# Performance work log

Hardware: AMD Instinct MI355X
Metric: run time of the kernel (lower is better)

The kernel has to match this reference:

```python
import jax, jax.numpy as jnp
import numpy as np

N_TOKENS = 131072
N_E = 1024
E_DIM = 256
BETA = 0.25
GAMMA = 0.99


def setup_inputs() -> dict:
    key = jax.random.key(0)
    k1, k2 = jax.random.split(key)
    z = jax.random.normal(k1, (N_TOKENS, E_DIM), dtype=jnp.float32)
    # nn.Embedding weight init: uniform(-1/n_e, 1/n_e)
    emb_weight = jax.random.uniform(k2, (N_E, E_DIM), dtype=jnp.float32,
                                    minval=-1.0 / N_E, maxval=1.0 / N_E)
    n_mat = jnp.ones((1, N_E), dtype=jnp.float32)
    m_mat = jnp.ones((N_E, E_DIM), dtype=jnp.float32)
    return {"z": z, "emb_weight": emb_weight, "n_mat": n_mat, "m_mat": m_mat,
            "batch_size": 128, "n_train": 100000}


def reference(z, emb_weight, n_mat, m_mat, batch_size, n_train):
    n_e, e_dim = emb_weight.shape
    zf = z.reshape(-1, e_dim)  # (N, e_dim)

    # squared-distance matrix: ||z||^2 + ||e||^2 - 2 z e^T  -> (N, n_e)
    d = (jnp.sum(zf * zf, axis=1, keepdims=True)
         + jnp.sum(emb_weight * emb_weight, axis=1)
         - 2.0 * (zf @ emb_weight.T))
    idx = jnp.argmin(d, axis=1)                       # (N,)
    min_encodings = jax.nn.one_hot(idx, n_e, dtype=z.dtype)  # (N, n_e)

    # z_q = one_hot @ weight == gather
    z_q = emb_weight[idx].reshape(z.shape)

    # EMA codebook update (the Python per-codeword loop == segment reductions)
    counts = jnp.sum(min_encodings, axis=0)           # (n_e,)
    new_n_mat = n_mat * GAMMA + counts[None, :] * (1.0 - GAMMA)
    sums = jax.ops.segment_sum(zf, idx, num_segments=n_e)  # (n_e, e_dim)
    new_m_mat = GAMMA * m_mat + (1.0 - GAMMA) * sums
    new_emb_weight = new_m_mat / new_n_mat[0][:, None]

    commit_loss = BETA * jnp.mean((jax.lax.stop_gradient(z_q) - z) ** 2)
    quant_loss = jnp.mean((z_q - jax.lax.stop_gradient(z)) ** 2)
    z_q_st = z + jax.lax.stop_gradient(z_q - z)       # straight-through

    e_mean = counts / zf.shape[0]
    perplexity = jnp.exp(-jnp.sum(e_mean * jnp.log(e_mean + 1e-10)))

    return (quant_loss, commit_loss, z_q_st, perplexity, min_encodings,
            idx[:, None], new_emb_weight, new_n_mat, new_m_mat)
```

## Files before the change

### kernel.cpp

```cpp
#include <hip/hip_runtime.h>


#define NT 131072
#define NE 1024
#define ED 256

typedef _Float16 f16;
typedef f16  f16x8 __attribute__((ext_vector_type(8)));
typedef float f32x4 __attribute__((ext_vector_type(4)));

static const size_t OFF_QL   = 0;
static const size_t OFF_CL   = 1;
static const size_t OFF_ZQ   = 2;
static const size_t OFF_PPL  = 33554434ULL;
static const size_t OFF_OH   = 33554435ULL;
static const size_t OFF_IDX  = 167772163ULL;
static const size_t OFF_NEMB = 167903235ULL;
static const size_t OFF_NN   = 168165379ULL;
static const size_t OFF_NM   = 168166403ULL;

__device__ __forceinline__ void gload_lds16(const void* g, void* l) {
  __builtin_amdgcn_global_load_lds(
      (const __attribute__((address_space(1))) unsigned int*)g,
      (__attribute__((address_space(3))) unsigned int*)l, 16, 0, 0);
}

__global__ __launch_bounds__(256) void rownorm_k(const float* __restrict__ x,
                                                 float* __restrict__ o, int nrows) {
  int wid  = blockIdx.x * 4 + (threadIdx.x >> 6);
  int lane = threadIdx.x & 63;
  if (wid >= nrows) return;
  float4 v = ((const float4*)(x + (size_t)wid * ED))[lane];
  float s = v.x * v.x + v.y * v.y + v.z * v.z + v.w * v.w;
  #pragma unroll
  for (int off = 32; off; off >>= 1) s += __shfl_down(s, off, 64);
  if (lane == 0) o[wid] = s;
}

__global__ __launch_bounds__(256) void eprep_k(const float* __restrict__ emb,
                                               char* __restrict__ eswz) {
  const int t  = threadIdx.x;
  const int c  = blockIdx.x * 8 + (t >> 5);
  const int kq = t & 31;
  const float* er = emb + (size_t)c * ED + kq * 8;
  float4 v0 = ((const float4*)er)[0];
  float4 v1 = ((const float4*)er)[1];
  float vv[8] = {v0.x, v0.y, v0.z, v0.w, v1.x, v1.y, v1.z, v1.w};
  f16x8 h;
  #pragma unroll
  for (int i = 0; i < 8; ++i) h[i] = (f16)(vv[i] * 1024.0f);
  const int tile = c >> 5, cl = c & 31;
  const int g = (cl << 5) | (kq ^ (cl & 7));
  *(f16x8*)(eswz + (size_t)tile * 16384 + (size_t)g * 16) = h;
}

__global__ __launch_bounds__(256, 2) void argmin_coarse_k(
    const float* __restrict__ z, const char* __restrict__ eswz,
    const float* __restrict__ enorm, int* __restrict__ idxw,
    int* __restrict__ nflag, int* __restrict__ flaglist) {
  __shared__ uint4 ebuf[2][1024];

  const int tid  = threadIdx.x;
  const int w    = tid >> 6, lane = tid & 63;
  const int lr   = lane & 15, kg = lane >> 4;
  const int r0   = blockIdx.x * 128 + w * 32;

  f16x8 ah[2][8];
  #pragma unroll
  for (int mf = 0; mf < 2; ++mf) {
    const float* zr = z + (size_t)(r0 + mf * 16 + lr) * ED + kg * 8;
    #pragma unroll
    for (int kt = 0; kt < 8; ++kt) {
      float4 a = ((const float4*)(zr + kt * 32))[0];
      float4 b = ((const float4*)(zr + kt * 32))[1];
      float vv[8] = {a.x, a.y, a.z, a.w, b.x, b.y, b.z, b.w};
      #pragma unroll
      for (int i = 0; i < 8; ++i) ah[mf][kt][i] = (f16)vv[i];
    }
  }

  float m1[2][4], m2[2][4]; int i1[2][4];
  #pragma unroll
  for (int mf = 0; mf < 2; ++mf)
    #pragma unroll
    for (int r = 0; r < 4; ++r) {
      m1[mf][r] = 3.4028235e38f; m2[mf][r] = 3.4028235e38f; i1[mf][r] = 0;
    }

  const int soff = w * 4096 + lane * 16;
  #pragma unroll
  for (int c = 0; c < 4; ++c)
    gload_lds16(eswz + soff + c * 1024,
                (char*)ebuf[0] + w * 4096 + c * 1024);
  __syncthreads();

  for (int ct = 0; ct < 32; ++ct) {
    const int cur = ct & 1;
    if (ct < 31) {
      const char* ntb = eswz + (size_t)(ct + 1) * 16384 + soff;
      #pragma unroll
      for (int c = 0; c < 4; ++c)
        gload_lds16(ntb + c * 1024,
                    (char*)ebuf[cur ^ 1] + w * 4096 + c * 1024);
    }
    const char* eb = (const char*)ebuf[cur];

    f32x4 acc[2][2];
    #pragma unroll
    for (int mf = 0; mf < 2; ++mf)
      #pragma unroll
      for (int nf = 0; nf < 2; ++nf) acc[mf][nf] = (f32x4){0.f, 0.f, 0.f, 0.f};

    #pragma unroll
    for (int kt = 0; kt < 8; ++kt) {
      f16x8 b0, b1;
      #pragma unroll
      for (int nf = 0; nf < 2; ++nf) {
        const int cl = nf * 16 + lr;
        const int kq = kt * 4 + kg;
        const int u  = (cl << 5) | (kq ^ (cl & 7));
        f16x8 bv = *(const f16x8*)(eb + u * 16);
        if (nf == 0) b0 = bv; else b1 = bv;
      }
      acc[0][0] = __builtin_amdgcn_mfma_f32_16x16x32_f16(ah[0][kt], b0, acc[0][0], 0, 0, 0);
      acc[1][0] = __builtin_amdgcn_mfma_f32_16x16x32_f16(ah[1][kt], b0, acc[1][0], 0, 0, 0);
      acc[0][1] = __builtin_amdgcn_mfma_f32_16x16x32_f16(ah[0][kt], b1, acc[0][1], 0, 0, 0);
      acc[1][1] = __builtin_amdgcn_mfma_f32_16x16x32_f16(ah[1][kt], b1, acc[1][1], 0, 0, 0);
    }

    #pragma unroll
    for (int nf = 0; nf < 2; ++nf) {
      const int c = ct * 32 + nf * 16 + lr;
      const float en = enorm[c];
      #pragma unroll
      for (int mf = 0; mf < 2; ++mf)
        #pragma unroll
        for (int r = 0; r < 4; ++r) {
          float dd = en - 0.001953125f * acc[mf][nf][r];
          if (dd < m1[mf][r]) {
            m2[mf][r] = m1[mf][r]; m1[mf][r] = dd; i1[mf][r] = c;
          } else if (dd < m2[mf][r]) {
            m2[mf][r] = dd;
          }
        }
    }
    __syncthreads();
  }

  #pragma unroll
  for (int mf = 0; mf < 2; ++mf)
    #pragma unroll
    for (int r = 0; r < 4; ++r) {
      float a1 = m1[mf][r]; int ai = i1[mf][r]; float a2 = m2[mf][r];
      #pragma unroll
      for (int off = 1; off < 16; off <<= 1) {
        float o1 = __shfl_xor(a1, off, 64);
        int   oi = __shfl_xor(ai, off, 64);
        float o2 = __shfl_xor(a2, off, 64);
        if (o1 < a1) { a2 = fminf(a1, o2); a1 = o1; ai = oi; }
        else         { a2 = fminf(a2, o1); }
      }
      if (lr == 0) {
        const int row = r0 + mf * 16 + kg * 4 + r;
        idxw[row] = ai;
        if (a2 - a1 < 4.0e-4f) {
          int p = atomicAdd(nflag, 1);
          flaglist[p] = row;
        }
      }
    }
}

__global__ __launch_bounds__(256) void argmin_refine_k(
    const float* __restrict__ z, const float* __restrict__ emb,
    const float* __restrict__ znorm, const float* __restrict__ enorm,
    const int* __restrict__ nflag, const int* __restrict__ flaglist,
    int* __restrict__ idxw) {
  const int nf = *nflag;
  const int b0 = blockIdx.x * 16;
  if (b0 >= nf) return;

  __shared__ float zl[16][256];
  __shared__ int   toks[16];
  __shared__ float rv[4][16];
  __shared__ int   ri[4][16];

  const int t = threadIdx.x;
  if (t < 16) {
    int li = b0 + t;
    toks[t] = flaglist[li < nf ? li : b0];
  }
  __syncthreads();

  #pragma unroll
  for (int i = 0; i < 4; ++i) {
    int li = t + i * 256;
    int row = li >> 6, c4 = li & 63;
    float4 v = ((const float4*)(z + (size_t)toks[row] * ED))[c4];
    *(float4*)&zl[row][c4 * 4] = v;
  }
  __syncthreads();

  float acc[4][16];
  #pragma unroll
  for (int cc = 0; cc < 4; ++cc)
    #pragma unroll
    for (int tk = 0; tk < 16; ++tk) acc[cc][tk] = 0.f;

  for (int c4 = 0; c4 < 64; ++c4) {
    float4 e[4];
    #pragma unroll
    for (int cc = 0; cc < 4; ++cc)
      e[cc] = ((const float4*)(emb + (size_t)(t * 4 + cc) * ED))[c4];
    #pragma unroll
    for (int tk = 0; tk < 16; ++tk) {
      float4 zv = *(const float4*)&zl[tk][c4 * 4];
      #pragma unroll
      for (int cc = 0; cc < 4; ++cc) {
        acc[cc][tk] += zv.x * e[cc].x;
        acc[cc][tk] += zv.y * e[cc].y;
        acc[cc][tk] += zv.z * e[cc].z;
        acc[cc][tk] += zv.w * e[cc].w;
      }
    }
  }

  float en[4];
  #pragma unroll
  for (int cc = 0; cc < 4; ++cc) en[cc] = enorm[t * 4 + cc];

  const int wv = t >> 6, lane = t & 63;
  for (int tk = 0; tk < 16; ++tk) {
    const float zn = znorm[toks[tk]];
    float bv = 3.4028235e38f; int bi = 0;
    #pragma unroll
    for (int cc = 0; cc < 4; ++cc) {
      float s = zn + en[cc];
      float d = s - 2.0f * acc[cc][tk];
      int   c = t * 4 + cc;
      if (d < bv) { bv = d; bi = c; }
    }
    #pragma unroll
    for (int off = 32; off; off >>= 1) {
      float ov = __shfl_down(bv, off, 64);
      int   oi = __shfl_down(bi, off, 64);
      if (ov < bv || (ov == bv && oi < bi)) { bv = ov; bi = oi; }
    }
    if (lane == 0) { rv[wv][tk] = bv; ri[wv][tk] = bi; }
  }
  __syncthreads();
  if (t < 16) {
    float bv = rv[0][t]; int bi = ri[0][t];
    #pragma unroll
    for (int wq = 1; wq < 4; ++wq) {
      float ov = rv[wq][t]; int oi = ri[wq][t];
      if (ov < bv || (ov == bv && oi < bi)) { bv = ov; bi = oi; }
    }
    idxw[toks[t]] = bi;
  }
}

__global__ __launch_bounds__(256) void zq_oh_k(
    const float* __restrict__ z, const float* __restrict__ emb,
    const int* __restrict__ idxw, float* __restrict__ out,
    double* __restrict__ lossacc) {
  const int t = threadIdx.x;
  const int tl = t >> 6, lane = t & 63;
  const int tok = blockIdx.x * 4 + tl;
  const int id = idxw[tok];

  float4 z4 = ((const float4*)(z   + (size_t)tok * ED))[lane];
  float4 e4 = ((const float4*)(emb + (size_t)id  * ED))[lane];
  float4 q;
  q.x = z4.x + (e4.x - z4.x);
  q.y = z4.y + (e4.y - z4.y);
  q.z = z4.z + (e4.z - z4.z);
  q.w = z4.w + (e4.w - z4.w);
  __builtin_memcpy(out + OFF_ZQ + (size_t)tok * ED + (size_t)lane * 4, &q, 16);

  float dx = e4.x - z4.x, dy = e4.y - z4.y, dz = e4.z - z4.z, dw = e4.w - z4.w;
  double lsum = (double)(dx * dx) + (double)(dy * dy)
              + (double)(dz * dz) + (double)(dw * dw);

  float* ohb = out + OFF_OH + (size_t)tok * NE;
  #pragma unroll
  for (int it = 0; it < 4; ++it) {
    int f4i = it * 64 + lane;
    int c0 = f4i * 4;
    float v[4];
    v[0] = (c0 + 0 == id) ? 1.0f : 0.0f;
    v[1] = (c0 + 1 == id) ? 1.0f : 0.0f;
    v[2] = (c0 + 2 == id) ? 1.0f : 0.0f;
    v[3] = (c0 + 3 == id) ? 1.0f : 0.0f;
    __builtin_memcpy(ohb + (size_t)f4i * 4, v, 16);
  }

  #pragma unroll
  for (int off = 32; off; off >>= 1) lsum += __shfl_down(lsum, off, 64);
  __shared__ double lred[4];
  if (lane == 0) lred[tl] = lsum;
  __syncthreads();
  if (t == 0)
    unsafeAtomicAdd(&lossacc[blockIdx.x & 255],
                    lred[0] + lred[1] + lred[2] + lred[3]);
}

__global__ __launch_bounds__(256) void hist_k(const int* __restrict__ idxw,
                                              int* __restrict__ counts) {
  __shared__ int lc[NE];
  for (int i = threadIdx.x; i < NE; i += 256) lc[i] = 0;
  __syncthreads();
  const int stride = gridDim.x * 256;
  for (int i = blockIdx.x * 256 + threadIdx.x; i < NT; i += stride)
    atomicAdd(&lc[idxw[i]], 1);
  __syncthreads();
  for (int i = threadIdx.x; i < NE; i += 256) {
    int v = lc[i];
    if (v) atomicAdd(&counts[i], v);
  }
}

__global__ __launch_bounds__(256) void scan_k(const int* __restrict__ counts,
                                              int* __restrict__ offsets) {
  const int t = threadIdx.x;
  const int lane = t & 63, w = t >> 6;
  int4 c = ((const int4*)counts)[t];
  int s = c.x + c.y + c.z + c.w;
  int v = s;
  #pragma unroll
  for (int off = 1; off < 64; off <<= 1) {
    int u = __shfl_up(v, off, 64);
    if (lane >= off) v += u;
  }
  __shared__ int wsum[4];
  if (lane == 63) wsum[w] = v;
  __syncthreads();
  int base = 0;
  #pragma unroll
  for (int i = 0; i < 4; ++i) if (i < w) base += wsum[i];
  int excl = base + v - s;
  int4 o;
  o.x = excl;
  o.y = o.x + c.x;
  o.z = o.y + c.y;
  o.w = o.z + c.z;
  ((int4*)offsets)[t] = o;
}

__global__ __launch_bounds__(256) void scatter_k(
    const int* __restrict__ idxw, const int* __restrict__ offsets,
    int* __restrict__ cursor, int* __restrict__ bucket,
    float* __restrict__ out) {
  int i = blockIdx.x * 256 + threadIdx.x;
  int id = idxw[i];
  out[OFF_IDX + i] = (float)id;
  int pos = atomicAdd(&cursor[id], 1);
  bucket[offsets[id] + pos] = i;
}

__global__ __launch_bounds__(256) void segsum_k(
    const float* __restrict__ z, const float* __restrict__ nmat,
    const float* __restrict__ mmat, const int* __restrict__ counts,
    const int* __restrict__ offsets, const int* __restrict__ bucket,
    float* __restrict__ out) {
  const int j = blockIdx.x, t = threadIdx.x;
  const int cnt = counts[j], off = offsets[j];
  float s = 0.f;
  int i = 0;
  for (; i + 4 <= cnt; i += 4) {
    int t0 = bucket[off + i + 0], t1 = bucket[off + i + 1];
    int t2 = bucket[off + i + 2], t3 = bucket[off + i + 3];
    float a = z[(size_t)t0 * ED + t];
    float b = z[(size_t)t1 * ED + t];
    float c = z[(size_t)t2 * ED + t];
    float d = z[(size_t)t3 * ED + t];
    s += a; s += b; s += c; s += d;
  }
  for (; i < cnt; ++i) s += z[(size_t)bucket[off + i] * ED + t];

  float newn = nmat[j] * 0.99f + (float)cnt * 0.01f;
  if (t == 0) out[OFF_NN + j] = newn;
  const size_t o = (size_t)j * ED + t;
  float newm = 0.99f * mmat[o] + 0.01f * s;
  out[OFF_NM + o]   = newm;
  out[OFF_NEMB + o] = newm / newn;
}

__global__ __launch_bounds__(256) void scalars_k(
    const double* __restrict__ lossacc, const int* __restrict__ counts,
    float* __restrict__ out) {
  const int t = threadIdx.x;
  double lsum = lossacc[t];
  double h = 0.0;
  for (int c = t; c < NE; c += 256) {
    double e = (double)counts[c] / (double)NT;
    h += e * log(e + 1e-10);
  }
  #pragma unroll
  for (int off = 32; off; off >>= 1) {
    lsum += __shfl_down(lsum, off, 64);
    h    += __shfl_down(h,    off, 64);
  }
  __shared__ double sl[4], sh[4];
  if ((t & 63) == 0) { sl[t >> 6] = lsum; sh[t >> 6] = h; }
  __syncthreads();
  if (t == 0) {
    double mean = (sl[0] + sl[1] + sl[2] + sl[3]) / (double)((size_t)NT * ED);
    out[OFF_QL]  = (float)mean;
    out[OFF_CL]  = (float)(0.25 * mean);
    out[OFF_PPL] = (float)exp(-(sh[0] + sh[1] + sh[2] + sh[3]));
  }
}

extern "C" void kernel_launch(void* const* d_in, const int* in_sizes, int n_in,
                              void* d_out, int out_size, void* d_ws, size_t ws_size,
                              hipStream_t stream) {
  const float* z    = (const float*)d_in[0];
  const float* emb  = (const float*)d_in[1];
  const float* nmat = (const float*)d_in[2];
  const float* mmat = (const float*)d_in[3];
  float* out = (float*)d_out;
  char*  ws  = (char*)d_ws;

  double* lossacc = (double*)ws;
  int*    nflag   = (int*)(ws + 2048);
  int*    counts  = (int*)(ws + 4096);
  int*    cursor  = (int*)(ws + 8192);
  int*    offsets = (int*)(ws + 12288);
  int*    bucket  = (int*)(ws + 16384);
  int*    idxw    = (int*)(ws + 540672);
  float*  znorm   = (float*)(ws + 1064960);
  float*  enorm   = (float*)(ws + 1589248);
  char*   eswz    = ws + 1593344;
  int*    flaglist= (int*)(ws + 2117632);

  hipMemsetAsync(ws, 0, 12288, stream);

  hipLaunchKernelGGL(rownorm_k, dim3(NT / 4), dim3(256), 0, stream, z, znorm, NT);
  hipLaunchKernelGGL(rownorm_k, dim3(NE / 4), dim3(256), 0, stream, emb, enorm, NE);
  hipLaunchKernelGGL(eprep_k, dim3(NE / 8), dim3(256), 0, stream, emb, eswz);
  hipLaunchKernelGGL(argmin_coarse_k, dim3(NT / 128), dim3(256), 0, stream,
                     z, eswz, enorm, idxw, nflag, flaglist);
  hipLaunchKernelGGL(argmin_refine_k, dim3(NT / 16), dim3(256), 0, stream,
                     z, emb, znorm, enorm, nflag, flaglist, idxw);
  hipLaunchKernelGGL(zq_oh_k, dim3(NT / 4), dim3(256), 0, stream,
                     z, emb, idxw, out, lossacc);
  hipLaunchKernelGGL(hist_k, dim3(64), dim3(256), 0, stream, idxw, counts);
  hipLaunchKernelGGL(scan_k, dim3(1), dim3(256), 0, stream, counts, offsets);
  hipLaunchKernelGGL(scatter_k, dim3(NT / 256), dim3(256), 0, stream,
                     idxw, offsets, cursor, bucket, out);
  hipLaunchKernelGGL(segsum_k, dim3(NE), dim3(256), 0, stream,
                     z, nmat, mmat, counts, offsets, bucket, out);
  hipLaunchKernelGGL(scalars_k, dim3(1), dim3(256), 0, stream,
                     lossacc, counts, out);
}
```

Baseline: 1.259 ms.

## Align z_q and one-hot stores, aggregate flag atomics per block

The output buffer offsets for z_q (2 floats) and one-hot (odd float offset) are not 16-byte aligned, so memcpy stores were likely split into scalar writes. The z_q store now shifts data across lanes with shuffles and the one-hot store is offset by one element, so that most lanes issue aligned float4 stores and only the edge elements use scalar writes. Separately, the coarse argmin kernel collects flagged rows in LDS and does one global atomic per block instead of one per row. Its launch bound changes from 2 to 1 blocks per SM, which may alter register allocation and occupancy.

```diff
diff --git a/kernel.cpp b/kernel.cpp
--- a/kernel.cpp
+++ b/kernel.cpp
@@ -54,16 +54,19 @@
   *(f16x8*)(eswz + (size_t)tile * 16384 + (size_t)g * 16) = h;
 }
 
-__global__ __launch_bounds__(256, 2) void argmin_coarse_k(
+__global__ __launch_bounds__(256, 1) void argmin_coarse_k(
     const float* __restrict__ z, const char* __restrict__ eswz,
     const float* __restrict__ enorm, int* __restrict__ idxw,
     int* __restrict__ nflag, int* __restrict__ flaglist) {
   __shared__ uint4 ebuf[2][1024];
+  __shared__ int   fcnt, fbase;
+  __shared__ int   frow[128];
 
   const int tid  = threadIdx.x;
   const int w    = tid >> 6, lane = tid & 63;
   const int lr   = lane & 15, kg = lane >> 4;
   const int r0   = blockIdx.x * 128 + w * 32;
+  if (tid == 0) fcnt = 0;
 
   f16x8 ah[2][8];
   #pragma unroll
@@ -164,11 +167,15 @@
         const int row = r0 + mf * 16 + kg * 4 + r;
         idxw[row] = ai;
         if (a2 - a1 < 4.0e-4f) {
-          int p = atomicAdd(nflag, 1);
-          flaglist[p] = row;
+          int p = atomicAdd(&fcnt, 1);
+          frow[p] = row;
         }
       }
     }
+  __syncthreads();
+  if (tid == 0 && fcnt > 0) fbase = atomicAdd(nflag, fcnt);
+  __syncthreads();
+  for (int i = tid; i < fcnt; i += 256) flaglist[fbase + i] = frow[i];
 }
 
 __global__ __launch_bounds__(256) void argmin_refine_k(
@@ -276,23 +283,37 @@
   q.y = z4.y + (e4.y - z4.y);
   q.z = z4.z + (e4.z - z4.z);
   q.w = z4.w + (e4.w - z4.w);
-  __builtin_memcpy(out + OFF_ZQ + (size_t)tok * ED + (size_t)lane * 4, &q, 16);
+
+  float* zb = out + OFF_ZQ + (size_t)tok * ED;
+  float nx = __shfl_down(q.x, 1, 64);
+  float ny = __shfl_down(q.y, 1, 64);
+  if (lane == 0) { zb[0] = q.x; zb[1] = q.y; }
+  if (lane < 63) {
+    float4 sv; sv.x = q.z; sv.y = q.w; sv.z = nx; sv.w = ny;
+    ((float4*)(zb + 2))[lane] = sv;
+  } else {
+    zb[254] = q.z; zb[255] = q.w;
+  }
 
   float dx = e4.x - z4.x, dy = e4.y - z4.y, dz = e4.z - z4.z, dw = e4.w - z4.w;
   double lsum = (double)(dx * dx) + (double)(dy * dy)
               + (double)(dz * dz) + (double)(dw * dw);
 
   float* ohb = out + OFF_OH + (size_t)tok * NE;
+  if (lane == 0) ohb[0] = (id == 0) ? 1.0f : 0.0f;
+  if (lane < 3)  ohb[1021 + lane] = (id == 1021 + lane) ? 1.0f : 0.0f;
   #pragma unroll
   for (int it = 0; it < 4; ++it) {
-    int f4i = it * 64 + lane;
-    int c0 = f4i * 4;
-    float v[4];
-    v[0] = (c0 + 0 == id) ? 1.0f : 0.0f;
-    v[1] = (c0 + 1 == id) ? 1.0f : 0.0f;
-    v[2] = (c0 + 2 == id) ? 1.0f : 0.0f;
-    v[3] = (c0 + 3 == id) ? 1.0f : 0.0f;
-    __builtin_memcpy(ohb + (size_t)f4i * 4, v, 16);
+    int j = it * 64 + lane;
+    if (j < 255) {
+      int c0 = 1 + 4 * j;
+      float4 v;
+      v.x = (c0 + 0 == id) ? 1.0f : 0.0f;
+      v.y = (c0 + 1 == id) ? 1.0f : 0.0f;
+      v.z = (c0 + 2 == id) ? 1.0f : 0.0f;
+      v.w = (c0 + 3 == id) ? 1.0f : 0.0f;
+      ((float4*)(ohb + 1))[j] = v;
+    }
   }
 
   #pragma unroll
```

New measurement: 1.236 ms. Within noise of the previous version (-1.8%).
